# Kernel tuning notes

Measured on AMD Instinct MI355X. Metric: run time of the kernel, lower is better.

## Reference

```python
import jax, jax.numpy as jnp
import numpy as np

NUM_HEADS = 16
EPS = 1e-12  # matches F.normalize eps


def _l2norm(x):
    return x / jnp.maximum(jnp.linalg.norm(x, axis=-1, keepdims=True), EPS)


def setup_inputs() -> dict:
    key = jax.random.key(0)
    ks = jax.random.split(key, 8)
    B, S, E, M = 2, 2048, 1024, 16384
    sc = 0.02
    return {
        "hidden_states": jax.random.normal(ks[0], (B, S, E), jnp.float32),
        "memory_keys": jax.random.normal(ks[1], (M, E), jnp.float32),
        "memory_values": jax.random.normal(ks[2], (M, E), jnp.float32),
        "Wq": jax.random.normal(ks[3], (E, E), jnp.float32) * sc,
        "bq": jnp.zeros((E,), jnp.float32),
        "Wk": jax.random.normal(ks[4], (E, E), jnp.float32) * sc,
        "bk": jnp.zeros((E,), jnp.float32),
        "Wv": jax.random.normal(ks[5], (E, E), jnp.float32) * sc,
        "bv": jnp.zeros((E,), jnp.float32),
        "Wo": jax.random.normal(ks[6], (E, E), jnp.float32) * sc,
        "bo": jnp.zeros((E,), jnp.float32),
        "top_k": 8,
    }


def reference(hidden_states, memory_keys, memory_values, Wq, bq, Wk, bk, Wv, bv, Wo, bo, top_k):
    B, S, E = hidden_states.shape
    H = NUM_HEADS
    hd = E // H
    scale = 1.0 / jnp.sqrt(jnp.float32(hd))

    def heads(x):  # [B,S,E] -> [B,H,S,hd]
        return x.reshape(B, S, H, hd).transpose(0, 2, 1, 3)

    q = heads(hidden_states @ Wq.T + bq)
    k = heads(hidden_states @ Wk.T + bk)
    v = heads(hidden_states @ Wv.T + bv)

    # self-attention scores [B,H,S,S]
    scores = jnp.einsum('bhqd,bhkd->bhqk', q, k) * scale

    # memory retrieval: cosine sim of raw hidden states vs memory keys
    qn = _l2norm(hidden_states)           # [B,S,E]
    kn = _l2norm(memory_keys)             # [M,E]
    sims = jnp.einsum('bse,me->bsm', qn, kn)   # [B,S,M]
    top_vals, top_idx = jax.lax.top_k(sims, top_k)  # [B,S,K]
    retrieved = memory_values[top_idx]    # [B,S,K,E] gather
    ret_h = retrieved.reshape(B, S, top_k, H, hd).transpose(0, 3, 1, 2, 4)  # [B,H,S,K,hd]

    # concat retrieval similarities as extra attention columns, re-softmax
    mem_scores = jnp.broadcast_to(top_vals[:, None, :, :], (B, H, S, top_k))
    ext = jnp.concatenate([scores, mem_scores], axis=-1)   # [B,H,S,S+K]
    probs = jax.nn.softmax(ext, axis=-1)

    ctx = jnp.einsum('bhqk,bhkd->bhqd', probs[..., :S], v)
    ctx = ctx + jnp.einsum('bhqk,bhqkd->bhqd', probs[..., S:], ret_h)

    ctx = ctx.transpose(0, 2, 1, 3).reshape(B, S, E)
    return ctx @ Wo.T + bo
```

## Files before the change

### kernel.cpp

```cpp
#include <hip/hip_runtime.h>
#include <math.h>

#define R_TOT 4096
#define E_DIM 1024
#define M_DIM 16384
#define H_NUM 16
#define HD    64
#define SEQ   2048
#define BATCH 2
#define TOPK  8
#define MIDK  16
#define NCHUNK 16
#define SCHUNK 1024
#define CANDS  32

typedef __attribute__((ext_vector_type(8))) short short8_t;
typedef __attribute__((ext_vector_type(4))) float f32x4;

__device__ inline unsigned short f2bf(float x) {
  unsigned u = __float_as_uint(x);
  u = (u + 0x7fff + ((u >> 16) & 1)) >> 16;
  return (unsigned short)u;
}
__device__ inline float bf2f(unsigned short h) {
  return __uint_as_float(((unsigned)h) << 16);
}

#define GLDS16(gp, lp) __builtin_amdgcn_global_load_lds( \
    (const __attribute__((address_space(1))) void*)(gp), \
    (__attribute__((address_space(3))) void*)(lp), 16, 0, 0)

__global__ __launch_bounds__(256) void norm_bf16_kernel(const float* __restrict__ X,
                                                        unsigned short* __restrict__ Y,
                                                        unsigned short* __restrict__ Yraw,
                                                        float* __restrict__ rinv_out) {
  int row = blockIdx.x;
  int tid = threadIdx.x;
  const float4* xr = (const float4*)(X + (size_t)row * E_DIM);
  float4 v = xr[tid];
  float s = v.x*v.x + v.y*v.y + v.z*v.z + v.w*v.w;
  #pragma unroll
  for (int off = 32; off; off >>= 1) s += __shfl_down(s, off, 64);
  __shared__ float wsum[4];
  if ((tid & 63) == 0) wsum[tid >> 6] = s;
  __syncthreads();
  float tot = wsum[0] + wsum[1] + wsum[2] + wsum[3];
  float rinv = 1.0f / fmaxf(sqrtf(tot), 1e-12f);
  if (tid == 0) rinv_out[row] = rinv;
  ushort4 o;
  o.x = f2bf(v.x * rinv); o.y = f2bf(v.y * rinv);
  o.z = f2bf(v.z * rinv); o.w = f2bf(v.w * rinv);
  ((ushort4*)(Y + (size_t)row * E_DIM))[tid] = o;
  if (Yraw) {
    ushort4 o2;
    o2.x = f2bf(v.x); o2.y = f2bf(v.y); o2.z = f2bf(v.z); o2.w = f2bf(v.w);
    ((ushort4*)(Yraw + (size_t)row * E_DIM))[tid] = o2;
  }
}

__global__ __launch_bounds__(256) void cast_bf16_kernel(const float* __restrict__ X,
                                                        unsigned short* __restrict__ Y, int n4) {
  int i = blockIdx.x * 256 + threadIdx.x;
  if (i < n4) {
    float4 v = ((const float4*)X)[i];
    ushort4 o;
    o.x = f2bf(v.x); o.y = f2bf(v.y); o.z = f2bf(v.z); o.w = f2bf(v.w);
    ((ushort4*)Y)[i] = o;
  }
}

template<int OUT_BF16>
__device__ __forceinline__ void gemm_tile_body(
    const unsigned short* __restrict__ Ab, const unsigned short* __restrict__ Bb,
    const float* __restrict__ bias, void* __restrict__ C, int N,
    int bm, int bn, char* pool) {
  short* Ap = (short*)pool;
  short* Bp = (short*)(pool + 16384);
  int tid = threadIdx.x;
  int wave = tid >> 6, lane = tid & 63;
  int wr = wave >> 1, wc = wave & 1;
  int li8 = lane >> 3;
  int gslot = (lane & 7) ^ li8;

  f32x4 acc[4][4];
  #pragma unroll
  for (int i = 0; i < 4; ++i)
    #pragma unroll
    for (int j = 0; j < 4; ++j)
      acc[i][j] = (f32x4){0.f, 0.f, 0.f, 0.f};

  for (int k0 = 0; k0 < E_DIM; k0 += 64) {
    #pragma unroll
    for (int s4 = 0; s4 < 8; ++s4) {
      int s = wave * 8 + s4;
      const unsigned short* gp;
      if (s < 16) {
        int r = s * 8 + li8;
        gp = Ab + (size_t)(bm + r) * E_DIM + k0 + gslot * 8;
      } else {
        int r = (s - 16) * 8 + li8;
        gp = Bb + (size_t)(bn + r) * E_DIM + k0 + gslot * 8;
      }
      GLDS16(gp, pool + s * 1024);
    }
    __syncthreads();
    #pragma unroll
    for (int ks = 0; ks < 2; ++ks) {
      short8_t af[4], bf[4];
      int kslot = ks * 4 + (lane >> 4);
      #pragma unroll
      for (int mi = 0; mi < 4; ++mi) {
        int r = wr * 64 + mi * 16 + (lane & 15);
        af[mi] = *(const short8_t*)(Ap + r * 64 + ((kslot ^ (r & 7)) * 8));
      }
      #pragma unroll
      for (int ni = 0; ni < 4; ++ni) {
        int r = wc * 64 + ni * 16 + (lane & 15);
        bf[ni] = *(const short8_t*)(Bp + r * 64 + ((kslot ^ (r & 7)) * 8));
      }
      #pragma unroll
      for (int mi = 0; mi < 4; ++mi)
        #pragma unroll
        for (int ni = 0; ni < 4; ++ni)
          acc[mi][ni] = __builtin_amdgcn_mfma_f32_16x16x32_bf16(af[mi], bf[ni], acc[mi][ni], 0, 0, 0);
    }
    __syncthreads();
  }
  #pragma unroll
  for (int mi = 0; mi < 4; ++mi) {
    #pragma unroll
    for (int ni = 0; ni < 4; ++ni) {
      int col = bn + wc * 64 + ni * 16 + (lane & 15);
      float bv = bias[col];
      #pragma unroll
      for (int r = 0; r < 4; ++r) {
        int row = bm + wr * 64 + mi * 16 + (lane >> 4) * 4 + r;
        float v = acc[mi][ni][r] + bv;
        if (OUT_BF16)
          ((unsigned short*)C)[(size_t)row * N + col] = f2bf(v);
        else
          ((float*)C)[(size_t)row * N + col] = v;
      }
    }
  }
}

__global__ __launch_bounds__(256) void mfma_gemm_out(
    const unsigned short* __restrict__ Ab, const unsigned short* __restrict__ Bb,
    const float* __restrict__ bias, float* __restrict__ C) {
  __shared__ __align__(16) char pool[32768];
  gemm_tile_body<0>(Ab, Bb, bias, C, E_DIM, blockIdx.x * 128, blockIdx.y * 128, pool);
}

__global__ __launch_bounds__(256) void mfma_gemm_qkv(
    const unsigned short* __restrict__ hb,
    const unsigned short* __restrict__ wq, const unsigned short* __restrict__ wk,
    const unsigned short* __restrict__ wv,
    const float* __restrict__ bq, const float* __restrict__ bk, const float* __restrict__ bv,
    unsigned short* __restrict__ q_b, unsigned short* __restrict__ k_b,
    unsigned short* __restrict__ v_b) {
  __shared__ __align__(16) char pool[32768];
  int bn_g = blockIdx.y * 128;
  int sel = bn_g >> 10;
  int bn = bn_g & 1023;
  const unsigned short* Bb = (sel == 0) ? wq : (sel == 1) ? wk : wv;
  const float* bias = (sel == 0) ? bq : (sel == 1) ? bk : bv;
  unsigned short* C = (sel == 0) ? q_b : (sel == 1) ? k_b : v_b;
  gemm_tile_body<1>(hb, Bb, bias, C, E_DIM, blockIdx.x * 128, bn, pool);
}

__global__ __launch_bounds__(256) void vtrans_kernel(const unsigned short* __restrict__ vb,
                                                     unsigned short* __restrict__ vT) {
  int st = blockIdx.x;
  int bh = blockIdx.y;
  int b = bh >> 4, h = bh & 15;
  __shared__ short T[64][72];
  int tid = threadIdx.x;
  #pragma unroll
  for (int it = 0; it < 2; ++it) {
    int idx = tid + it * 256;
    int r = idx >> 3, sl = idx & 7;
    short8_t v = *(const short8_t*)(vb + ((size_t)(b * SEQ + st * 64 + r)) * E_DIM + h * HD + sl * 8);
    *(short8_t*)&T[r][sl * 8] = v;
  }
  __syncthreads();
  int d = tid >> 2, sp = (tid & 3) * 16;
  short8_t o0, o1;
  #pragma unroll
  for (int u = 0; u < 8; ++u) o0[u] = T[sp + u][d];
  #pragma unroll
  for (int u = 0; u < 8; ++u) o1[u] = T[sp + 8 + u][d];
  size_t base = ((size_t)bh * HD + d) * SEQ + st * 64 + sp;
  *(short8_t*)(vT + base) = o0;
  *(short8_t*)(vT + base + 8) = o1;
}

#define SPITCH 132

__global__ __launch_bounds__(512) void sims_topk_kernel(
    const unsigned short* __restrict__ Hn, const unsigned short* __restrict__ MKn,
    float* __restrict__ cand_v, int* __restrict__ cand_i) {
  __shared__ __align__(16) char pool[33792];
  short* Ap = (short*)pool;
  short* Bp = (short*)(pool + 16384);
  short* Sp = (short*)pool;

  int bm = blockIdx.x * 128;
  int chunk = blockIdx.y;
  int tid = threadIdx.x;
  int wave = tid >> 6, lane = tid & 63;
  int wr = wave >> 2, wc = wave & 3;
  int srow = tid >> 2, sl = tid & 3;
  int li8 = lane >> 3;
  int gslot = (lane & 7) ^ li8;

  float tv[TOPK]; int ti[TOPK];
  #pragma unroll
  for (int u = 0; u < TOPK; ++u) { tv[u] = -INFINITY; ti[u] = 0; }

  for (int sub = 0; sub < SCHUNK / 128; ++sub) {
    int bn = chunk * SCHUNK + sub * 128;
    f32x4 acc[4][2];
    #pragma unroll
    for (int i = 0; i < 4; ++i)
      #pragma unroll
      for (int j = 0; j < 2; ++j)
        acc[i][j] = (f32x4){0.f, 0.f, 0.f, 0.f};

    for (int k0 = 0; k0 < E_DIM; k0 += 64) {
      #pragma unroll
      for (int s4 = 0; s4 < 4; ++s4) {
        int s = wave * 4 + s4;
        const unsigned short* gp;
        if (s < 16) {
          int r = s * 8 + li8;
          gp = Hn + (size_t)(bm + r) * E_DIM + k0 + gslot * 8;
        } else {
          int r = (s - 16) * 8 + li8;
          gp = MKn + (size_t)(bn + r) * E_DIM + k0 + gslot * 8;
        }
        GLDS16(gp, pool + s * 1024);
      }
      __syncthreads();
      #pragma unroll
      for (int ks = 0; ks < 2; ++ks) {
        short8_t af[4], bf[2];
        int kslot = ks * 4 + (lane >> 4);
        #pragma unroll
        for (int mi = 0; mi < 4; ++mi) {
          int r = wr * 64 + mi * 16 + (lane & 15);
          af[mi] = *(const short8_t*)(Ap + r * 64 + ((kslot ^ (r & 7)) * 8));
        }
        #pragma unroll
        for (int ni = 0; ni < 2; ++ni) {
          int r = wc * 32 + ni * 16 + (lane & 15);
          bf[ni] = *(const short8_t*)(Bp + r * 64 + ((kslot ^ (r & 7)) * 8));
        }
        #pragma unroll
        for (int mi = 0; mi < 4; ++mi)
          #pragma unroll
          for (int ni = 0; ni < 2; ++ni)
            acc[mi][ni] = __builtin_amdgcn_mfma_f32_16x16x32_bf16(af[mi], bf[ni], acc[mi][ni], 0, 0, 0);
      }
      __syncthreads();
    }
    #pragma unroll
    for (int mi = 0; mi < 4; ++mi) {
      #pragma unroll
      for (int ni = 0; ni < 2; ++ni) {
        int scol = wc * 32 + ni * 16 + (lane & 15);
        #pragma unroll
        for (int r = 0; r < 4; ++r) {
          int srw = wr * 64 + mi * 16 + (lane >> 4) * 4 + r;
          Sp[srw * SPITCH + scol] = (short)f2bf(acc[mi][ni][r]);
        }
      }
    }
    __syncthreads();
    #pragma unroll
    for (int u4 = 0; u4 < 8; ++u4) {
      const short* p = Sp + srow * SPITCH + sl * 32 + u4 * 4;
      short4 v4 = *(const short4*)p;
      short vv[4] = {v4.x, v4.y, v4.z, v4.w};
      #pragma unroll
      for (int j = 0; j < 4; ++j) {
        float v = bf2f((unsigned short)vv[j]);
        if (v > tv[0]) {
          int idx = bn + sl * 32 + u4 * 4 + j;
          int p_ = 0;
          #pragma unroll
          for (int q = 1; q < TOPK; ++q)
            if (v > tv[q]) { tv[q-1] = tv[q]; ti[q-1] = ti[q]; p_ = q; }
          tv[p_] = v; ti[p_] = idx;
        }
      }
    }
    __syncthreads();
  }
  size_t base = (((size_t)(bm + srow)) * NCHUNK + chunk) * CANDS + sl * TOPK;
  #pragma unroll
  for (int u = 0; u < TOPK; ++u) { cand_v[base + u] = tv[u]; cand_i[base + u] = ti[u]; }
}

__global__ __launch_bounds__(64) void merge_topk_kernel(
    const float* __restrict__ cand_v, const int* __restrict__ cand_i,
    int* __restrict__ mid_i) {
  int row = blockIdx.x;
  int lane = threadIdx.x;
  size_t base = (size_t)row * (NCHUNK * CANDS);
  float v[8]; int id[8];
  #pragma unroll
  for (int u = 0; u < 8; ++u) {
    v[u]  = cand_v[base + lane*8 + u];
    id[u] = cand_i[base + lane*8 + u];
  }
  for (int t = 0; t < MIDK; ++t) {
    float bvv = v[0]; int bu = 0;
    #pragma unroll
    for (int u = 1; u < 8; ++u) if (v[u] > bvv) { bvv = v[u]; bu = u; }
    float mv = bvv; int ml = lane;
    #pragma unroll
    for (int off = 32; off; off >>= 1) {
      float ov = __shfl_down(mv, off, 64);
      int   ol = __shfl_down(ml, off, 64);
      if (ov > mv) { mv = ov; ml = ol; }
    }
    ml = __shfl(ml, 0, 64);
    if (lane == ml) {
      mid_i[(size_t)row * MIDK + t] = id[bu];
      v[bu] = -INFINITY;
    }
  }
}

__global__ __launch_bounds__(256) void refine_kernel(
    const float* __restrict__ hidden, const float* __restrict__ mkeys,
    const float* __restrict__ rinvH, const float* __restrict__ rinvK,
    const int* __restrict__ mid_i,
    float* __restrict__ top_v, int* __restrict__ top_i) {
  int row = blockIdx.x;
  int tid = threadIdx.x;
  int wave = tid >> 6, lane = tid & 63;
  __shared__ float hrow[E_DIM];
  __shared__ float rv[MIDK];
  __shared__ int   ri[MIDK];
  ((float4*)hrow)[tid] = ((const float4*)(hidden + (size_t)row * E_DIM))[tid];
  __syncthreads();
  float rh = rinvH[row];
  for (int c = wave; c < MIDK; c += 4) {
    int idx = mid_i[(size_t)row * MIDK + c];
    const float* kp = mkeys + (size_t)idx * E_DIM;
    float s = 0.f;
    #pragma unroll
    for (int rr = 0; rr < 4; ++rr) {
      float4 kv = *(const float4*)(kp + rr * 256 + lane * 4);
      float4 hv = *(const float4*)(hrow + rr * 256 + lane * 4);
      s += hv.x*kv.x + hv.y*kv.y + hv.z*kv.z + hv.w*kv.w;
    }
    #pragma unroll
    for (int off = 32; off; off >>= 1) s += __shfl_down(s, off, 64);
    if (lane == 0) { rv[c] = s * rh * rinvK[idx]; ri[c] = idx; }
  }
  __syncthreads();
  if (tid == 0) {
    bool used[MIDK] = {};
    #pragma unroll
    for (int t = 0; t < TOPK; ++t) {
      float best = -INFINITY; int bi = -1; int bidx = 0x7fffffff;
      for (int c = 0; c < MIDK; ++c) {
        if (used[c]) continue;
        if (rv[c] > best || (rv[c] == best && ri[c] < bidx)) {
          best = rv[c]; bi = c; bidx = ri[c];
        }
      }
      used[bi] = true;
      top_v[(size_t)row * TOPK + t] = best;
      top_i[(size_t)row * TOPK + t] = bidx;
    }
  }
}

__global__ __launch_bounds__(256) void flash_mfma_kernel(
    const unsigned short* __restrict__ qb, const unsigned short* __restrict__ kb,
    const unsigned short* __restrict__ vT, const float* __restrict__ MV,
    const float* __restrict__ top_v, const int* __restrict__ top_i,
    unsigned short* __restrict__ ctx) {
  __shared__ __align__(16) char pool[32768];
  short* Kp = (short*)pool;
  short* Vp = (short*)(pool + 8192);
  int qt = blockIdx.x;
  int bh = blockIdx.y;
  int b = bh >> 4, h = bh & 15;
  int tid = threadIdx.x;
  int wave = tid >> 6, lane = tid & 63;
  int g = lane >> 4, c = lane & 15;
  int li8 = lane >> 3;
  int gslot = (lane & 7) ^ li8;
  short* Pw = (short*)(pool + 16384 + wave * 4096);
  const float scale = 0.125f;

  short8_t aQ[2][2];
  #pragma unroll
  for (int mi = 0; mi < 2; ++mi)
    #pragma unroll
    for (int ks = 0; ks < 2; ++ks) {
      size_t row = (size_t)b * SEQ + qt * 128 + wave * 32 + mi * 16 + c;
      aQ[mi][ks] = *(const short8_t*)(qb + row * E_DIM + h * HD + (ks * 4 + g) * 8);
    }

  f32x4 oa[2][4];
  #pragma unroll
  for (int mi = 0; mi < 2; ++mi)
    #pragma unroll
    for (int nd = 0; nd < 4; ++nd)
      oa[mi][nd] = (f32x4){0.f, 0.f, 0.f, 0.f};
  float m_[2][4], l_[2][4];
  #pragma unroll
  for (int mi = 0; mi < 2; ++mi)
    #pragma unroll
    for (int r = 0; r < 4; ++r) { m_[mi][r] = -INFINITY; l_[mi][r] = 0.f; }

  for (int kv0 = 0; kv0 < SEQ; kv0 += 64) {
    #pragma unroll
    for (int j = 0; j < 4; ++j) {
      int s = wave * 4 + j;
      const unsigned short* gp;
      if (s < 8) {
        int r = s * 8 + li8;
        gp = kb + ((size_t)(b * SEQ + kv0 + r)) * E_DIM + h * HD + gslot * 8;
      } else {
        int d = (s - 8) * 8 + li8;
        gp = vT + ((size_t)(bh * HD + d)) * SEQ + kv0 + gslot * 8;
      }
      GLDS16(gp, pool + s * 1024);
    }
    __syncthreads();

    f32x4 sa[2][4];
    #pragma unroll
    for (int mi = 0; mi < 2; ++mi)
      #pragma unroll
      for (int ni = 0; ni < 4; ++ni)
        sa[mi][ni] = (f32x4){0.f, 0.f, 0.f, 0.f};
    #pragma unroll
    for (int ks = 0; ks < 2; ++ks) {
      short8_t bK[4];
      #pragma unroll
      for (int ni = 0; ni < 4; ++ni) {
        int r = ni * 16 + c;
        bK[ni] = *(const short8_t*)(Kp + r * 64 + (((ks * 4 + g) ^ (r & 7)) * 8));
      }
      #pragma unroll
      for (int mi = 0; mi < 2; ++mi)
        #pragma unroll
        for (int ni = 0; ni < 4; ++ni)
          sa[mi][ni] = __builtin_amdgcn_mfma_f32_16x16x32_bf16(aQ[mi][ks], bK[ni], sa[mi][ni], 0, 0, 0);
    }
    #pragma unroll
    for (int mi = 0; mi < 2; ++mi)
      #pragma unroll
      for (int ni = 0; ni < 4; ++ni)
        #pragma unroll
        for (int r = 0; r < 4; ++r)
          sa[mi][ni][r] *= scale;
    float fsc[2][4];
    #pragma unroll
    for (int mi = 0; mi < 2; ++mi)
      #pragma unroll
      for (int r = 0; r < 4; ++r) {
        float m0 = fmaxf(fmaxf(sa[mi][0][r], sa[mi][1][r]), fmaxf(sa[mi][2][r], sa[mi][3][r]));
        #pragma unroll
        for (int off = 1; off < 16; off <<= 1) m0 = fmaxf(m0, __shfl_xor(m0, off, 64));
        float mn = fmaxf(m_[mi][r], m0);
        fsc[mi][r] = __expf(m_[mi][r] - mn);
        m_[mi][r] = mn;
      }
    #pragma unroll
    for (int mi = 0; mi < 2; ++mi)
      #pragma unroll
      for (int nd = 0; nd < 4; ++nd)
        #pragma unroll
        for (int r = 0; r < 4; ++r)
          oa[mi][nd][r] *= fsc[mi][r];
    #pragma unroll
    for (int mi = 0; mi < 2; ++mi)
      #pragma unroll
      for (int r = 0; r < 4; ++r) {
        float ps = 0.f;
        #pragma unroll
        for (int ni = 0; ni < 4; ++ni) {
          float p = __expf(sa[mi][ni][r] - m_[mi][r]);
          sa[mi][ni][r] = p;
          ps += p;
        }
        #pragma unroll
        for (int off = 1; off < 16; off <<= 1) ps += __shfl_xor(ps, off, 64);
        l_[mi][r] = l_[mi][r] * fsc[mi][r] + ps;
      }
    #pragma unroll
    for (int mi = 0; mi < 2; ++mi)
      #pragma unroll
      for (int ni = 0; ni < 4; ++ni)
        #pragma unroll
        for (int r = 0; r < 4; ++r) {
          int ql = mi * 16 + g * 4 + r;
          int slot = (ni * 2 + (c >> 3)) ^ (ql & 7);
          Pw[ql * 64 + slot * 8 + (c & 7)] = (short)f2bf(sa[mi][ni][r]);
        }
    #pragma unroll
    for (int ks = 0; ks < 2; ++ks) {
      short8_t aP[2], bV[4];
      #pragma unroll
      for (int mi = 0; mi < 2; ++mi) {
        int ql = mi * 16 + c;
        aP[mi] = *(const short8_t*)(Pw + ql * 64 + (((ks * 4 + g) ^ (ql & 7)) * 8));
      }
      #pragma unroll
      for (int nd = 0; nd < 4; ++nd) {
        int dr = nd * 16 + c;
        bV[nd] = *(const short8_t*)(Vp + dr * 64 + (((ks * 4 + g) ^ (dr & 7)) * 8));
      }
      #pragma unroll
      for (int mi = 0; mi < 2; ++mi)
        #pragma unroll
        for (int nd = 0; nd < 4; ++nd)
          oa[mi][nd] = __builtin_amdgcn_mfma_f32_16x16x32_bf16(aP[mi], bV[nd], oa[mi][nd], 0, 0, 0);
    }
    __syncthreads();
  }

  #pragma unroll
  for (int mi = 0; mi < 2; ++mi)
    #pragma unroll
    for (int r = 0; r < 4; ++r) {
      size_t row = (size_t)b * SEQ + qt * 128 + wave * 32 + mi * 16 + g * 4 + r;
      const float* tvp = top_v + row * TOPK;
      const int*   tip = top_i + row * TOPK;
      float lg[TOPK];
      float mmax = m_[mi][r];
      #pragma unroll
      for (int j = 0; j < TOPK; ++j) { lg[j] = tvp[j]; mmax = fmaxf(mmax, lg[j]); }
      float f = __expf(m_[mi][r] - mmax);
      float l = l_[mi][r] * f;
      #pragma unroll
      for (int nd = 0; nd < 4; ++nd) oa[mi][nd][r] *= f;
      #pragma unroll
      for (int j = 0; j < TOPK; ++j) {
        float p = __expf(lg[j] - mmax);
        l += p;
        const float* mvp = MV + (size_t)tip[j] * E_DIM + h * HD + c;
        #pragma unroll
        for (int nd = 0; nd < 4; ++nd)
          oa[mi][nd][r] = fmaf(p, mvp[nd * 16], oa[mi][nd][r]);
      }
      float inv = 1.0f / l;
      #pragma unroll
      for (int nd = 0; nd < 4; ++nd)
        ctx[row * E_DIM + h * HD + nd * 16 + c] = f2bf(oa[mi][nd][r] * inv);
    }
}

extern "C" void kernel_launch(void* const* d_in, const int* in_sizes, int n_in,
                              void* d_out, int out_size, void* d_ws, size_t ws_size,
                              hipStream_t stream) {
  (void)in_sizes; (void)n_in; (void)out_size; (void)ws_size;
  const float* hidden = (const float*)d_in[0];
  const float* mkeys  = (const float*)d_in[1];
  const float* mvals  = (const float*)d_in[2];
  const float* Wq = (const float*)d_in[3];
  const float* bq = (const float*)d_in[4];
  const float* Wk = (const float*)d_in[5];
  const float* bk = (const float*)d_in[6];
  const float* Wv = (const float*)d_in[7];
  const float* bv = (const float*)d_in[8];
  const float* Wo = (const float*)d_in[9];
  const float* bo = (const float*)d_in[10];

  char* ws = (char*)d_ws;
  float* cand_v = (float*)ws;                                  ws += (size_t)R_TOT * NCHUNK * CANDS * 4;
  int*   cand_i = (int*)ws;                                    ws += (size_t)R_TOT * NCHUNK * CANDS * 4;
  int*   mid_i  = (int*)ws;                                    ws += (size_t)R_TOT * MIDK * 4;
  float* top_v  = (float*)ws;                                  ws += (size_t)R_TOT * TOPK * 4;
  int*   top_i  = (int*)ws;                                    ws += (size_t)R_TOT * TOPK * 4;
  float* rinvH  = (float*)ws;                                  ws += (size_t)R_TOT * 4;
  float* rinvK  = (float*)ws;                                  ws += (size_t)M_DIM * 4;
  unsigned short* Hn   = (unsigned short*)ws;                  ws += (size_t)R_TOT * E_DIM * 2;
  unsigned short* MKn  = (unsigned short*)ws;                  ws += (size_t)M_DIM * E_DIM * 2;
  unsigned short* hb   = (unsigned short*)ws;                  ws += (size_t)R_TOT * E_DIM * 2;
  unsigned short* wqb  = (unsigned short*)ws;                  ws += (size_t)E_DIM * E_DIM * 2;
  unsigned short* wkb  = (unsigned short*)ws;                  ws += (size_t)E_DIM * E_DIM * 2;
  unsigned short* wvb  = (unsigned short*)ws;                  ws += (size_t)E_DIM * E_DIM * 2;
  unsigned short* wob  = (unsigned short*)ws;                  ws += (size_t)E_DIM * E_DIM * 2;
  unsigned short* q_b  = (unsigned short*)ws;                  ws += (size_t)R_TOT * E_DIM * 2;
  unsigned short* k_b  = (unsigned short*)ws;                  ws += (size_t)R_TOT * E_DIM * 2;
  unsigned short* v_b  = (unsigned short*)ws;                  ws += (size_t)R_TOT * E_DIM * 2;
  unsigned short* vTb  = (unsigned short*)ws;                  ws += (size_t)R_TOT * E_DIM * 2;
  unsigned short* ctxb = (unsigned short*)ws;                  ws += (size_t)R_TOT * E_DIM * 2;

  norm_bf16_kernel<<<dim3(R_TOT), 256, 0, stream>>>(hidden, Hn, hb, rinvH);
  norm_bf16_kernel<<<dim3(M_DIM), 256, 0, stream>>>(mkeys, MKn, (unsigned short*)nullptr, rinvK);

  int n4w = E_DIM * E_DIM / 4;
  cast_bf16_kernel<<<dim3(n4w / 256), 256, 0, stream>>>(Wq, wqb, n4w);
  cast_bf16_kernel<<<dim3(n4w / 256), 256, 0, stream>>>(Wk, wkb, n4w);
  cast_bf16_kernel<<<dim3(n4w / 256), 256, 0, stream>>>(Wv, wvb, n4w);
  cast_bf16_kernel<<<dim3(n4w / 256), 256, 0, stream>>>(Wo, wob, n4w);

  mfma_gemm_qkv<<<dim3(R_TOT / 128, 3 * E_DIM / 128), 256, 0, stream>>>(
      hb, wqb, wkb, wvb, bq, bk, bv, q_b, k_b, v_b);

  vtrans_kernel<<<dim3(SEQ / 64, BATCH * H_NUM), 256, 0, stream>>>(v_b, vTb);

  sims_topk_kernel<<<dim3(R_TOT / 128, NCHUNK), 512, 0, stream>>>(Hn, MKn, cand_v, cand_i);
  merge_topk_kernel<<<dim3(R_TOT), 64, 0, stream>>>(cand_v, cand_i, mid_i);
  refine_kernel<<<dim3(R_TOT), 256, 0, stream>>>(hidden, mkeys, rinvH, rinvK, mid_i, top_v, top_i);

  flash_mfma_kernel<<<dim3(SEQ / 128, BATCH * H_NUM), 256, 0, stream>>>(
      q_b, k_b, vTb, mvals, top_v, top_i, ctxb);

  mfma_gemm_out<<<dim3(R_TOT / 128, E_DIM / 128), 256, 0, stream>>>(ctxb, wob, bo, (float*)d_out);
}
```

Before: 642.5 us.

## Double-buffer LDS tiles in sims/top-k GEMM to overlap loads with MFMA

Flattens the sub-tile and K loops of the similarity/top-k kernel into one step loop and double-buffers the A/B LDS tiles, so the next tile's global-to-LDS copy is issued before the MFMA work on the current tile. A partial vmcnt wait plus raw s_barrier replaces the full syncthreads. The score scratch gets its own LDS region, which raises LDS use from about 33KB to about 98KB per block and may cut occupancy. The top-k epilogue still runs every 16 steps with its own barriers.

```diff
diff --git a/kernel.cpp b/kernel.cpp
--- a/kernel.cpp
+++ b/kernel.cpp
@@ -196,14 +196,13 @@
 }
 
 #define SPITCH 132
+#define NSTEP (SCHUNK / 128 * 16)
 
 __global__ __launch_bounds__(512) void sims_topk_kernel(
     const unsigned short* __restrict__ Hn, const unsigned short* __restrict__ MKn,
     float* __restrict__ cand_v, int* __restrict__ cand_i) {
-  __shared__ __align__(16) char pool[33792];
-  short* Ap = (short*)pool;
-  short* Bp = (short*)(pool + 16384);
-  short* Sp = (short*)pool;
+  __shared__ __align__(16) char pool[65536 + 128 * SPITCH * 2];
+  short* Sp = (short*)(pool + 65536);
 
   int bm = blockIdx.x * 128;
   int chunk = blockIdx.y;
@@ -218,84 +217,106 @@
   #pragma unroll
   for (int u = 0; u < TOPK; ++u) { tv[u] = -INFINITY; ti[u] = 0; }
 
-  for (int sub = 0; sub < SCHUNK / 128; ++sub) {
+  auto STAGE = [&](int d, int t) {
+    int sub = t >> 4;
+    int k0 = (t & 15) * 64;
     int bn = chunk * SCHUNK + sub * 128;
-    f32x4 acc[4][2];
-    #pragma unroll
-    for (int i = 0; i < 4; ++i)
-      #pragma unroll
-      for (int j = 0; j < 2; ++j)
-        acc[i][j] = (f32x4){0.f, 0.f, 0.f, 0.f};
-
-    for (int k0 = 0; k0 < E_DIM; k0 += 64) {
-      #pragma unroll
-      for (int s4 = 0; s4 < 4; ++s4) {
-        int s = wave * 4 + s4;
-        const unsigned short* gp;
-        if (s < 16) {
-          int r = s * 8 + li8;
-          gp = Hn + (size_t)(bm + r) * E_DIM + k0 + gslot * 8;
-        } else {
-          int r = (s - 16) * 8 + li8;
-          gp = MKn + (size_t)(bn + r) * E_DIM + k0 + gslot * 8;
+    #pragma unroll
+    for (int s4 = 0; s4 < 4; ++s4) {
+      int s = wave * 4 + s4;
+      const unsigned short* gp;
+      if (s < 16) {
+        int r = s * 8 + li8;
+        gp = Hn + (size_t)(bm + r) * E_DIM + k0 + gslot * 8;
+      } else {
+        int r = (s - 16) * 8 + li8;
+        gp = MKn + (size_t)(bn + r) * E_DIM + k0 + gslot * 8;
+      }
+      GLDS16(gp, pool + d * 32768 + s * 1024);
+    }
+  };
+
+  f32x4 acc[4][2];
+  #pragma unroll
+  for (int i = 0; i < 4; ++i)
+    #pragma unroll
+    for (int j = 0; j < 2; ++j)
+      acc[i][j] = (f32x4){0.f, 0.f, 0.f, 0.f};
+
+  STAGE(0, 0);
+
+  for (int t = 0; t < NSTEP; ++t) {
+    int cur = t & 1;
+    if (t + 1 < NSTEP) {
+      STAGE(1 - cur, t + 1);
+      asm volatile("s_waitcnt vmcnt(4)" ::: "memory");
+    } else {
+      asm volatile("s_waitcnt vmcnt(0)" ::: "memory");
+    }
+    __builtin_amdgcn_s_barrier();
+    __builtin_amdgcn_sched_barrier(0);
+
+    short* Ap = (short*)(pool + cur * 32768);
+    short* Bp = (short*)(pool + cur * 32768 + 16384);
+    #pragma unroll
+    for (int ks = 0; ks < 2; ++ks) {
+      short8_t af[4], bf[2];
+      int kslot = ks * 4 + (lane >> 4);
+      #pragma unroll
+      for (int mi = 0; mi < 4; ++mi) {
+        int r = wr * 64 + mi * 16 + (lane & 15);
+        af[mi] = *(const short8_t*)(Ap + r * 64 + ((kslot ^ (r & 7)) * 8));
+      }
+      #pragma unroll
+      for (int ni = 0; ni < 2; ++ni) {
+        int r = wc * 32 + ni * 16 + (lane & 15);
+        bf[ni] = *(const short8_t*)(Bp + r * 64 + ((kslot ^ (r & 7)) * 8));
+      }
+      #pragma unroll
+      for (int mi = 0; mi < 4; ++mi)
+        #pragma unroll
+        for (int ni = 0; ni < 2; ++ni)
+          acc[mi][ni] = __builtin_amdgcn_mfma_f32_16x16x32_bf16(af[mi], bf[ni], acc[mi][ni], 0, 0, 0);
+    }
+    __builtin_amdgcn_sched_barrier(0);
+    __builtin_amdgcn_s_barrier();
+
+    if ((t & 15) == 15) {
+      int bn = chunk * SCHUNK + (t >> 4) * 128;
+      #pragma unroll
+      for (int mi = 0; mi < 4; ++mi) {
+        #pragma unroll
+        for (int ni = 0; ni < 2; ++ni) {
+          int scol = wc * 32 + ni * 16 + (lane & 15);
+          #pragma unroll
+          for (int r = 0; r < 4; ++r) {
+            int srw = wr * 64 + mi * 16 + (lane >> 4) * 4 + r;
+            Sp[srw * SPITCH + scol] = (short)f2bf(acc[mi][ni][r]);
+          }
+          acc[mi][ni] = (f32x4){0.f, 0.f, 0.f, 0.f};
         }
-        GLDS16(gp, pool + s * 1024);
       }
       __syncthreads();
       #pragma unroll
-      for (int ks = 0; ks < 2; ++ks) {
-        short8_t af[4], bf[2];
-        int kslot = ks * 4 + (lane >> 4);
-        #pragma unroll
-        for (int mi = 0; mi < 4; ++mi) {
-          int r = wr * 64 + mi * 16 + (lane & 15);
-          af[mi] = *(const short8_t*)(Ap + r * 64 + ((kslot ^ (r & 7)) * 8));
+      for (int u4 = 0; u4 < 8; ++u4) {
+        const short* p = Sp + srow * SPITCH + sl * 32 + u4 * 4;
+        short4 v4 = *(const short4*)p;
+        short vv[4] = {v4.x, v4.y, v4.z, v4.w};
+        #pragma unroll
+        for (int j = 0; j < 4; ++j) {
+          float v = bf2f((unsigned short)vv[j]);
+          if (v > tv[0]) {
+            int idx = bn + sl * 32 + u4 * 4 + j;
+            int p_ = 0;
+            #pragma unroll
+            for (int q = 1; q < TOPK; ++q)
+              if (v > tv[q]) { tv[q-1] = tv[q]; ti[q-1] = ti[q]; p_ = q; }
+            tv[p_] = v; ti[p_] = idx;
+          }
         }
-        #pragma unroll
-        for (int ni = 0; ni < 2; ++ni) {
-          int r = wc * 32 + ni * 16 + (lane & 15);
-          bf[ni] = *(const short8_t*)(Bp + r * 64 + ((kslot ^ (r & 7)) * 8));
-        }
-        #pragma unroll
-        for (int mi = 0; mi < 4; ++mi)
-          #pragma unroll
-          for (int ni = 0; ni < 2; ++ni)
-            acc[mi][ni] = __builtin_amdgcn_mfma_f32_16x16x32_bf16(af[mi], bf[ni], acc[mi][ni], 0, 0, 0);
       }
       __syncthreads();
     }
-    #pragma unroll
-    for (int mi = 0; mi < 4; ++mi) {
-      #pragma unroll
-      for (int ni = 0; ni < 2; ++ni) {
-        int scol = wc * 32 + ni * 16 + (lane & 15);
-        #pragma unroll
-        for (int r = 0; r < 4; ++r) {
-          int srw = wr * 64 + mi * 16 + (lane >> 4) * 4 + r;
-          Sp[srw * SPITCH + scol] = (short)f2bf(acc[mi][ni][r]);
-        }
-      }
-    }
-    __syncthreads();
-    #pragma unroll
-    for (int u4 = 0; u4 < 8; ++u4) {
-      const short* p = Sp + srow * SPITCH + sl * 32 + u4 * 4;
-      short4 v4 = *(const short4*)p;
-      short vv[4] = {v4.x, v4.y, v4.z, v4.w};
-      #pragma unroll
-      for (int j = 0; j < 4; ++j) {
-        float v = bf2f((unsigned short)vv[j]);
-        if (v > tv[0]) {
-          int idx = bn + sl * 32 + u4 * 4 + j;
-          int p_ = 0;
-          #pragma unroll
-          for (int q = 1; q < TOPK; ++q)
-            if (v > tv[q]) { tv[q-1] = tv[q]; ti[q-1] = ti[q]; p_ = q; }
-          tv[p_] = v; ti[p_] = idx;
-        }
-      }
-    }
-    __syncthreads();
   }
   size_t base = (((size_t)(bm + srow)) * NCHUNK + chunk) * CANDS + sl * TOPK;
   #pragma unroll
```

After: 575.0 us. -10.5%, faster.
